# Kernel optimization log

Hardware: AMD Instinct MI355X
Metric: run time of the kernel (lower is better)

## Reference

```python
import jax, jax.numpy as jnp
import numpy as np

C, B, N, IN, OUT = 10, 128, 1152, 8, 16  # num_capsules, batch, num_route_nodes, in_ch, out_ch
NUM_ITERS = 3


def squash(t):
    # t: [..., OUT]
    sq_norm = jnp.sum(t * t, axis=-1, keepdims=True)
    scale = sq_norm / (1.0 + sq_norm)
    return scale * t / jnp.sqrt(sq_norm + 1e-8)


def setup_inputs() -> dict:
    key = jax.random.key(0)
    k1, k2 = jax.random.split(key)
    x = jax.random.normal(k1, (B, N, IN), dtype=jnp.float32)
    route_weights = jax.random.normal(k2, (C, N, IN, OUT), dtype=jnp.float32)
    return {"x": x, "route_weights": route_weights}


def reference(x, route_weights):
    # priors[c,b,n,o] = sum_i x[b,n,i] * W[c,n,i,o]
    priors = jnp.einsum('bni,cnio->cbno', x, route_weights)  # [C,B,N,OUT]
    # torch: logits = zeros_like(priors[:, :, :, 0]) -> [C,B,N,OUT] (dim 3 was the
    # singleton matmul row dim, so the OUT axis survives on the logits)
    logits = jnp.zeros_like(priors)
    outputs = None
    for _ in range(NUM_ITERS):
        attn = jax.nn.softmax(logits, axis=2)            # over route nodes N
        outputs = squash(jnp.sum(attn * priors, axis=2))  # [C,B,OUT]
        # (outputs * priors).sum(-1) broadcasts to [C,B,N,1] added to [C,B,N,OUT]
        logits = logits + jnp.sum(outputs[:, :, None, :] * priors, axis=-1, keepdims=True)
    return outputs  # [C,B,OUT] == outputs.squeeze() in torch (B>1, C>1)
```

## Files before the change

kernel.cpp:

```cpp
#include <hip/hip_runtime.h>
#include <hip/hip_bf16.h>


constexpr int C = 10, B = 128, N = 1152, IN = 8, OUT = 16;
constexpr int THREADS = 512;
constexpr int NW = THREADS / 64;
constexpr int G = 2;
constexpr int PASSES = N / (NW * 16);
constexpr int NBLK = C * (B / G);
constexpr int NXCD = 8;
constexpr int CHUNK = NBLK / NXCD;

__device__ __forceinline__ unsigned packbf(float a, float b) {
    __hip_bfloat162 h = __float22bfloat162_rn(float2{a, b});
    return *(unsigned*)&h;
}
__device__ __forceinline__ float bflo(unsigned u) { return __uint_as_float(u << 16); }
__device__ __forceinline__ float bfhi(unsigned u) { return __uint_as_float(u & 0xffff0000u); }

__global__ __launch_bounds__(THREADS)
void caps_route(const float* __restrict__ Xf, const float* __restrict__ Wf,
                float* __restrict__ Of) {
    __shared__ uint2 ldsP[G * PASSES * THREADS];
    __shared__ float lds_s[2][G][NW][OUT];
    __shared__ float lds_sum[2][G][NW];

    const int t = threadIdx.x;
    const int l = t & 63;
    const int wid = t >> 6;
    const int q = l & 3;
    const int rsub = l >> 2;

    const int bid = blockIdx.x;
    const int blk = (bid & (NXCD - 1)) * CHUNK + (bid >> 3);
    const int c = blk >> 6;
    const int b0 = (blk & 63) * G;

    #pragma unroll
    for (int p = 0; p < PASSES; ++p) {
        const int n = wid * (16 * PASSES) + p * 16 + rsub;
        const float4* wr = (const float4*)(Wf + (size_t)(c * N + n) * (IN * OUT));
        float4 wv[IN];
        #pragma unroll
        for (int i = 0; i < IN; ++i) wv[i] = wr[i * 4 + q];
        #pragma unroll
        for (int g = 0; g < G; ++g) {
            const float4* xr = (const float4*)(Xf + (size_t)((b0 + g) * N + n) * IN);
            const float4 xa = xr[0], xc = xr[1];
            const float xs[8] = { xa.x, xa.y, xa.z, xa.w, xc.x, xc.y, xc.z, xc.w };
            float a0 = 0.f, a1 = 0.f, a2 = 0.f, a3 = 0.f;
            #pragma unroll
            for (int i = 0; i < IN; ++i) {
                a0 = fmaf(xs[i], wv[i].x, a0);
                a1 = fmaf(xs[i], wv[i].y, a1);
                a2 = fmaf(xs[i], wv[i].z, a2);
                a3 = fmaf(xs[i], wv[i].w, a3);
            }
            ldsP[(g * PASSES + p) * THREADS + t] =
                uint2{packbf(a0, a1), packbf(a2, a3)};
        }
    }

    float oa[G][4];
    #pragma unroll
    for (int g = 0; g < G; ++g)
        #pragma unroll
        for (int k = 0; k < 4; ++k) oa[g][k] = 0.f;

    for (int it = 0; it < 3; ++it) {
        const int pb = it & 1;
        float s4[G][4];
        float ssum[G];
        if (it == 0) {
            #pragma unroll
            for (int g = 0; g < G; ++g) {
                ssum[g] = (float)PASSES;
                float a0 = 0.f, a1 = 0.f, a2 = 0.f, a3 = 0.f;
                #pragma unroll
                for (int p = 0; p < PASSES; ++p) {
                    const uint2 u = ldsP[(g * PASSES + p) * THREADS + t];
                    a0 += bflo(u.x); a1 += bfhi(u.x);
                    a2 += bflo(u.y); a3 += bfhi(u.y);
                }
                s4[g][0] = a0; s4[g][1] = a1; s4[g][2] = a2; s4[g][3] = a3;
            }
        } else {
            #pragma unroll
            for (int g = 0; g < G; ++g) {
                ssum[g] = 0.f;
                #pragma unroll
                for (int k = 0; k < 4; ++k) s4[g][k] = 0.f;
                #pragma unroll
                for (int p = 0; p < PASSES; ++p) {
                    const uint2 u = ldsP[(g * PASSES + p) * THREADS + t];
                    const float p0 = bflo(u.x), p1 = bfhi(u.x);
                    const float p2 = bflo(u.y), p3 = bfhi(u.y);
                    float d = oa[g][0] * p0;
                    d = fmaf(oa[g][1], p1, d);
                    d = fmaf(oa[g][2], p2, d);
                    d = fmaf(oa[g][3], p3, d);
                    d += __shfl_xor(d, 1, 64);
                    d += __shfl_xor(d, 2, 64);
                    const float e = __expf(d);
                    ssum[g] += e;
                    s4[g][0] = fmaf(e, p0, s4[g][0]);
                    s4[g][1] = fmaf(e, p1, s4[g][1]);
                    s4[g][2] = fmaf(e, p2, s4[g][2]);
                    s4[g][3] = fmaf(e, p3, s4[g][3]);
                }
            }
        }
        #pragma unroll
        for (int m = 4; m < 64; m <<= 1) {
            #pragma unroll
            for (int g = 0; g < G; ++g) {
                ssum[g] += __shfl_xor(ssum[g], m, 64);
                #pragma unroll
                for (int k = 0; k < 4; ++k) s4[g][k] += __shfl_xor(s4[g][k], m, 64);
            }
        }
        if (l < 4) {
            #pragma unroll
            for (int g = 0; g < G; ++g)
                #pragma unroll
                for (int k = 0; k < 4; ++k) lds_s[pb][g][wid][l * 4 + k] = s4[g][k];
        }
        if (l == 0) {
            #pragma unroll
            for (int g = 0; g < G; ++g) lds_sum[pb][g][wid] = ssum[g];
        }
        __syncthreads();

        float ov[G][4];
        #pragma unroll
        for (int g = 0; g < G; ++g) {
            float a0 = 0.f, a1 = 0.f, a2 = 0.f, a3 = 0.f, S = 0.f;
            #pragma unroll
            for (int w = 0; w < NW; ++w) {
                const float4 v = *(const float4*)&lds_s[pb][g][w][q * 4];
                a0 += v.x; a1 += v.y; a2 += v.z; a3 += v.w;
                S += lds_sum[pb][g][w];
            }
            const float inv = 1.f / S;
            const float s0 = a0 * inv, s1 = a1 * inv;
            const float s2 = a2 * inv, s3 = a3 * inv;
            float r = s0 * s0 + s1 * s1 + s2 * s2 + s3 * s3;
            r += __shfl_xor(r, 1, 64);
            r += __shfl_xor(r, 2, 64);
            const float sc = r / ((1.f + r) * sqrtf(r + 1e-8f));
            ov[g][0] = s0 * sc; ov[g][1] = s1 * sc;
            ov[g][2] = s2 * sc; ov[g][3] = s3 * sc;
        }
        if (it < 2) {
            #pragma unroll
            for (int g = 0; g < G; ++g)
                #pragma unroll
                for (int k = 0; k < 4; ++k) oa[g][k] += ov[g][k];
        } else if (t < 4) {
            #pragma unroll
            for (int g = 0; g < G; ++g)
                #pragma unroll
                for (int k = 0; k < 4; ++k)
                    Of[((size_t)c * B + b0 + g) * OUT + q * 4 + k] = ov[g][k];
        }
    }
}

extern "C" void kernel_launch(void* const* d_in, const int* in_sizes, int n_in,
                              void* d_out, int out_size, void* d_ws, size_t ws_size,
                              hipStream_t stream) {
    const float* X = (const float*)d_in[0];
    const float* W = (const float*)d_in[1];
    float* O = (float*)d_out;
    hipLaunchKernelGGL(caps_route, dim3(NBLK), dim3(THREADS), 0, stream, X, W, O);
}
```

Measured before the change: 94.95 us.

## Assign one batch element per block and fuse first-iteration sum into prior computation

Drops the two-batch-per-block grouping so each block handles one (capsule, batch) pair, doubling the grid and halving LDS per block. The first routing iteration's uniform sum is now accumulated in fp32 registers while priors are computed, so the LDS re-read pass is skipped. Launch bounds now request more resident blocks per CU. The trade-off is that each W row is loaded twice as often, once per batch element instead of once per pair.

After: 108.4 us. 1.14x slower.

```diff
diff --git a/kernel.cpp b/kernel.cpp
--- a/kernel.cpp
+++ b/kernel.cpp
@@ -5,9 +5,8 @@
 constexpr int C = 10, B = 128, N = 1152, IN = 8, OUT = 16;
 constexpr int THREADS = 512;
 constexpr int NW = THREADS / 64;
-constexpr int G = 2;
 constexpr int PASSES = N / (NW * 16);
-constexpr int NBLK = C * (B / G);
+constexpr int NBLK = C * B;
 constexpr int NXCD = 8;
 constexpr int CHUNK = NBLK / NXCD;
 
@@ -18,12 +17,12 @@
 __device__ __forceinline__ float bflo(unsigned u) { return __uint_as_float(u << 16); }
 __device__ __forceinline__ float bfhi(unsigned u) { return __uint_as_float(u & 0xffff0000u); }
 
-__global__ __launch_bounds__(THREADS)
+__global__ __launch_bounds__(THREADS, 8)
 void caps_route(const float* __restrict__ Xf, const float* __restrict__ Wf,
                 float* __restrict__ Of) {
-    __shared__ uint2 ldsP[G * PASSES * THREADS];
-    __shared__ float lds_s[2][G][NW][OUT];
-    __shared__ float lds_sum[2][G][NW];
+    __shared__ uint2 ldsP[PASSES * THREADS];
+    __shared__ float lds_s[2][NW][OUT];
+    __shared__ float lds_sum[2][NW];
 
     const int t = threadIdx.x;
     const int l = t & 63;
@@ -33,9 +32,10 @@
 
     const int bid = blockIdx.x;
     const int blk = (bid & (NXCD - 1)) * CHUNK + (bid >> 3);
-    const int c = blk >> 6;
-    const int b0 = (blk & 63) * G;
+    const int c = blk >> 7;
+    const int b = blk & 127;
 
+    float s40[4] = {0.f, 0.f, 0.f, 0.f};
     #pragma unroll
     for (int p = 0; p < PASSES; ++p) {
         const int n = wid * (16 * PASSES) + p * 16 + rsub;
@@ -43,125 +43,89 @@
         float4 wv[IN];
         #pragma unroll
         for (int i = 0; i < IN; ++i) wv[i] = wr[i * 4 + q];
+        const float4* xr = (const float4*)(Xf + (size_t)(b * N + n) * IN);
+        const float4 xa = xr[0], xc = xr[1];
+        const float xs[8] = { xa.x, xa.y, xa.z, xa.w, xc.x, xc.y, xc.z, xc.w };
+        float a0 = 0.f, a1 = 0.f, a2 = 0.f, a3 = 0.f;
         #pragma unroll
-        for (int g = 0; g < G; ++g) {
-            const float4* xr = (const float4*)(Xf + (size_t)((b0 + g) * N + n) * IN);
-            const float4 xa = xr[0], xc = xr[1];
-            const float xs[8] = { xa.x, xa.y, xa.z, xa.w, xc.x, xc.y, xc.z, xc.w };
-            float a0 = 0.f, a1 = 0.f, a2 = 0.f, a3 = 0.f;
-            #pragma unroll
-            for (int i = 0; i < IN; ++i) {
-                a0 = fmaf(xs[i], wv[i].x, a0);
-                a1 = fmaf(xs[i], wv[i].y, a1);
-                a2 = fmaf(xs[i], wv[i].z, a2);
-                a3 = fmaf(xs[i], wv[i].w, a3);
-            }
-            ldsP[(g * PASSES + p) * THREADS + t] =
-                uint2{packbf(a0, a1), packbf(a2, a3)};
+        for (int i = 0; i < IN; ++i) {
+            a0 = fmaf(xs[i], wv[i].x, a0);
+            a1 = fmaf(xs[i], wv[i].y, a1);
+            a2 = fmaf(xs[i], wv[i].z, a2);
+            a3 = fmaf(xs[i], wv[i].w, a3);
         }
+        s40[0] += a0; s40[1] += a1; s40[2] += a2; s40[3] += a3;
+        ldsP[p * THREADS + t] = uint2{packbf(a0, a1), packbf(a2, a3)};
     }
 
-    float oa[G][4];
-    #pragma unroll
-    for (int g = 0; g < G; ++g)
-        #pragma unroll
-        for (int k = 0; k < 4; ++k) oa[g][k] = 0.f;
+    float oa[4] = {0.f, 0.f, 0.f, 0.f};
 
     for (int it = 0; it < 3; ++it) {
         const int pb = it & 1;
-        float s4[G][4];
-        float ssum[G];
+        float s4[4];
+        float ssum;
         if (it == 0) {
+            ssum = (float)PASSES;
             #pragma unroll
-            for (int g = 0; g < G; ++g) {
-                ssum[g] = (float)PASSES;
-                float a0 = 0.f, a1 = 0.f, a2 = 0.f, a3 = 0.f;
-                #pragma unroll
-                for (int p = 0; p < PASSES; ++p) {
-                    const uint2 u = ldsP[(g * PASSES + p) * THREADS + t];
-                    a0 += bflo(u.x); a1 += bfhi(u.x);
-                    a2 += bflo(u.y); a3 += bfhi(u.y);
-                }
-                s4[g][0] = a0; s4[g][1] = a1; s4[g][2] = a2; s4[g][3] = a3;
-            }
+            for (int k = 0; k < 4; ++k) s4[k] = s40[k];
         } else {
+            ssum = 0.f;
             #pragma unroll
-            for (int g = 0; g < G; ++g) {
-                ssum[g] = 0.f;
-                #pragma unroll
-                for (int k = 0; k < 4; ++k) s4[g][k] = 0.f;
-                #pragma unroll
-                for (int p = 0; p < PASSES; ++p) {
-                    const uint2 u = ldsP[(g * PASSES + p) * THREADS + t];
-                    const float p0 = bflo(u.x), p1 = bfhi(u.x);
-                    const float p2 = bflo(u.y), p3 = bfhi(u.y);
-                    float d = oa[g][0] * p0;
-                    d = fmaf(oa[g][1], p1, d);
-                    d = fmaf(oa[g][2], p2, d);
-                    d = fmaf(oa[g][3], p3, d);
-                    d += __shfl_xor(d, 1, 64);
-                    d += __shfl_xor(d, 2, 64);
-                    const float e = __expf(d);
-                    ssum[g] += e;
-                    s4[g][0] = fmaf(e, p0, s4[g][0]);
-                    s4[g][1] = fmaf(e, p1, s4[g][1]);
-                    s4[g][2] = fmaf(e, p2, s4[g][2]);
-                    s4[g][3] = fmaf(e, p3, s4[g][3]);
-                }
+            for (int k = 0; k < 4; ++k) s4[k] = 0.f;
+            #pragma unroll
+            for (int p = 0; p < PASSES; ++p) {
+                const uint2 u = ldsP[p * THREADS + t];
+                const float p0 = bflo(u.x), p1 = bfhi(u.x);
+                const float p2 = bflo(u.y), p3 = bfhi(u.y);
+                float d = oa[0] * p0;
+                d = fmaf(oa[1], p1, d);
+                d = fmaf(oa[2], p2, d);
+                d = fmaf(oa[3], p3, d);
+                d += __shfl_xor(d, 1, 64);
+                d += __shfl_xor(d, 2, 64);
+                const float e = __expf(d);
+                ssum += e;
+                s4[0] = fmaf(e, p0, s4[0]);
+                s4[1] = fmaf(e, p1, s4[1]);
+                s4[2] = fmaf(e, p2, s4[2]);
+                s4[3] = fmaf(e, p3, s4[3]);
             }
         }
         #pragma unroll
         for (int m = 4; m < 64; m <<= 1) {
+            ssum += __shfl_xor(ssum, m, 64);
             #pragma unroll
-            for (int g = 0; g < G; ++g) {
-                ssum[g] += __shfl_xor(ssum[g], m, 64);
-                #pragma unroll
-                for (int k = 0; k < 4; ++k) s4[g][k] += __shfl_xor(s4[g][k], m, 64);
-            }
+            for (int k = 0; k < 4; ++k) s4[k] += __shfl_xor(s4[k], m, 64);
         }
         if (l < 4) {
             #pragma unroll
-            for (int g = 0; g < G; ++g)
-                #pragma unroll
-                for (int k = 0; k < 4; ++k) lds_s[pb][g][wid][l * 4 + k] = s4[g][k];
+            for (int k = 0; k < 4; ++k) lds_s[pb][wid][l * 4 + k] = s4[k];
         }
-        if (l == 0) {
-            #pragma unroll
-            for (int g = 0; g < G; ++g) lds_sum[pb][g][wid] = ssum[g];
-        }
+        if (l == 0) lds_sum[pb][wid] = ssum;
         __syncthreads();
 
-        float ov[G][4];
+        float a0 = 0.f, a1 = 0.f, a2 = 0.f, a3 = 0.f, S = 0.f;
         #pragma unroll
-        for (int g = 0; g < G; ++g) {
-            float a0 = 0.f, a1 = 0.f, a2 = 0.f, a3 = 0.f, S = 0.f;
-            #pragma unroll
-            for (int w = 0; w < NW; ++w) {
-                const float4 v = *(const float4*)&lds_s[pb][g][w][q * 4];
-                a0 += v.x; a1 += v.y; a2 += v.z; a3 += v.w;
-                S += lds_sum[pb][g][w];
-            }
-            const float inv = 1.f / S;
-            const float s0 = a0 * inv, s1 = a1 * inv;
-            const float s2 = a2 * inv, s3 = a3 * inv;
-            float r = s0 * s0 + s1 * s1 + s2 * s2 + s3 * s3;
-            r += __shfl_xor(r, 1, 64);
-            r += __shfl_xor(r, 2, 64);
-            const float sc = r / ((1.f + r) * sqrtf(r + 1e-8f));
-            ov[g][0] = s0 * sc; ov[g][1] = s1 * sc;
-            ov[g][2] = s2 * sc; ov[g][3] = s3 * sc;
+        for (int w = 0; w < NW; ++w) {
+            const float4 v = *(const float4*)&lds_s[pb][w][q * 4];
+            a0 += v.x; a1 += v.y; a2 += v.z; a3 += v.w;
+            S += lds_sum[pb][w];
         }
+        const float inv = 1.f / S;
+        const float s0 = a0 * inv, s1 = a1 * inv;
+        const float s2 = a2 * inv, s3 = a3 * inv;
+        float r = s0 * s0 + s1 * s1 + s2 * s2 + s3 * s3;
+        r += __shfl_xor(r, 1, 64);
+        r += __shfl_xor(r, 2, 64);
+        const float sc = r / ((1.f + r) * sqrtf(r + 1e-8f));
         if (it < 2) {
-            #pragma unroll
-            for (int g = 0; g < G; ++g)
-                #pragma unroll
-                for (int k = 0; k < 4; ++k) oa[g][k] += ov[g][k];
+            oa[0] += s0 * sc; oa[1] += s1 * sc;
+            oa[2] += s2 * sc; oa[3] += s3 * sc;
         } else if (t < 4) {
-            #pragma unroll
-            for (int g = 0; g < G; ++g)
-                #pragma unroll
-                for (int k = 0; k < 4; ++k)
-                    Of[((size_t)c * B + b0 + g) * OUT + q * 4 + k] = ov[g][k];
+            Of[((size_t)c * B + b) * OUT + q * 4 + 0] = s0 * sc;
+            Of[((size_t)c * B + b) * OUT + q * 4 + 1] = s1 * sc;
+            Of[((size_t)c * B + b) * OUT + q * 4 + 2] = s2 * sc;
+            Of[((size_t)c * B + b) * OUT + q * 4 + 3] = s3 * sc;
         }
     }
 }
```

## Use 1024-thread blocks with uneven row split and fused first-iteration sums

Applied to the files above, without the earlier changes.

Doubles the block size to 1024 threads (16 waves), so each wave now handles 72 route nodes in 4 or 5 row passes, with divergence on the last pass. The priors layout in LDS changes to node-major indexing. The first routing iteration's sums now come from fp32 accumulators during the priors computation, which skips one LDS re-read pass. The prior computation is also hand-interleaved for both batch rows and loads W in two halves to reduce register pressure. The risks are lower occupancy flexibility with 1024-thread blocks, divergence on the fifth pass, and a rolled loop.

After: 122.4 us. 1.29x slower.

```diff
diff --git a/kernel.cpp b/kernel.cpp
--- a/kernel.cpp
+++ b/kernel.cpp
@@ -3,10 +3,10 @@
 
 
 constexpr int C = 10, B = 128, N = 1152, IN = 8, OUT = 16;
-constexpr int THREADS = 512;
+constexpr int THREADS = 1024;
 constexpr int NW = THREADS / 64;
 constexpr int G = 2;
-constexpr int PASSES = N / (NW * 16);
+constexpr int ROWS_W = N / NW;
 constexpr int NBLK = C * (B / G);
 constexpr int NXCD = 8;
 constexpr int CHUNK = NBLK / NXCD;
@@ -21,7 +21,7 @@
 __global__ __launch_bounds__(THREADS)
 void caps_route(const float* __restrict__ Xf, const float* __restrict__ Wf,
                 float* __restrict__ Of) {
-    __shared__ uint2 ldsP[G * PASSES * THREADS];
+    __shared__ uint2 ldsP[G * N * 4];
     __shared__ float lds_s[2][G][NW][OUT];
     __shared__ float lds_sum[2][G][NW];
 
@@ -36,53 +36,70 @@
     const int c = blk >> 6;
     const int b0 = (blk & 63) * G;
 
-    #pragma unroll
-    for (int p = 0; p < PASSES; ++p) {
-        const int n = wid * (16 * PASSES) + p * 16 + rsub;
-        const float4* wr = (const float4*)(Wf + (size_t)(c * N + n) * (IN * OUT));
-        float4 wv[IN];
-        #pragma unroll
-        for (int i = 0; i < IN; ++i) wv[i] = wr[i * 4 + q];
-        #pragma unroll
-        for (int g = 0; g < G; ++g) {
-            const float4* xr = (const float4*)(Xf + (size_t)((b0 + g) * N + n) * IN);
-            const float4 xa = xr[0], xc = xr[1];
-            const float xs[8] = { xa.x, xa.y, xa.z, xa.w, xc.x, xc.y, xc.z, xc.w };
-            float a0 = 0.f, a1 = 0.f, a2 = 0.f, a3 = 0.f;
-            #pragma unroll
-            for (int i = 0; i < IN; ++i) {
-                a0 = fmaf(xs[i], wv[i].x, a0);
-                a1 = fmaf(xs[i], wv[i].y, a1);
-                a2 = fmaf(xs[i], wv[i].z, a2);
-                a3 = fmaf(xs[i], wv[i].w, a3);
-            }
-            ldsP[(g * PASSES + p) * THREADS + t] =
-                uint2{packbf(a0, a1), packbf(a2, a3)};
+    float s40[G][4] = {{0.f, 0.f, 0.f, 0.f}, {0.f, 0.f, 0.f, 0.f}};
+    const int nbase = wid * ROWS_W + rsub;
+    #pragma unroll 1
+    for (int p = 0; p < 5; ++p) {
+        if ((p < 4) | (rsub < 8)) {
+            const int n = nbase + p * 16;
+            const float4* wr = (const float4*)(Wf + (size_t)(c * N + n) * (IN * OUT)) + q;
+            const float4* x0 = (const float4*)(Xf + (size_t)((b0 + 0) * N + n) * IN);
+            const float4* x1 = (const float4*)(Xf + (size_t)((b0 + 1) * N + n) * IN);
+            const float4 xa0 = x0[0], xc0 = x0[1];
+            const float4 xa1 = x1[0], xc1 = x1[1];
+            float4 u0 = wr[0], u1 = wr[4], u2 = wr[8], u3 = wr[12];
+            float a0 = xa0.x * u0.x, a1 = xa0.x * u0.y, a2 = xa0.x * u0.z, a3 = xa0.x * u0.w;
+            float b0v = xa1.x * u0.x, b1v = xa1.x * u0.y, b2v = xa1.x * u0.z, b3v = xa1.x * u0.w;
+            a0 = fmaf(xa0.y, u1.x, a0); a1 = fmaf(xa0.y, u1.y, a1);
+            a2 = fmaf(xa0.y, u1.z, a2); a3 = fmaf(xa0.y, u1.w, a3);
+            b0v = fmaf(xa1.y, u1.x, b0v); b1v = fmaf(xa1.y, u1.y, b1v);
+            b2v = fmaf(xa1.y, u1.z, b2v); b3v = fmaf(xa1.y, u1.w, b3v);
+            a0 = fmaf(xa0.z, u2.x, a0); a1 = fmaf(xa0.z, u2.y, a1);
+            a2 = fmaf(xa0.z, u2.z, a2); a3 = fmaf(xa0.z, u2.w, a3);
+            b0v = fmaf(xa1.z, u2.x, b0v); b1v = fmaf(xa1.z, u2.y, b1v);
+            b2v = fmaf(xa1.z, u2.z, b2v); b3v = fmaf(xa1.z, u2.w, b3v);
+            a0 = fmaf(xa0.w, u3.x, a0); a1 = fmaf(xa0.w, u3.y, a1);
+            a2 = fmaf(xa0.w, u3.z, a2); a3 = fmaf(xa0.w, u3.w, a3);
+            b0v = fmaf(xa1.w, u3.x, b0v); b1v = fmaf(xa1.w, u3.y, b1v);
+            b2v = fmaf(xa1.w, u3.z, b2v); b3v = fmaf(xa1.w, u3.w, b3v);
+            u0 = wr[16]; u1 = wr[20]; u2 = wr[24]; u3 = wr[28];
+            a0 = fmaf(xc0.x, u0.x, a0); a1 = fmaf(xc0.x, u0.y, a1);
+            a2 = fmaf(xc0.x, u0.z, a2); a3 = fmaf(xc0.x, u0.w, a3);
+            b0v = fmaf(xc1.x, u0.x, b0v); b1v = fmaf(xc1.x, u0.y, b1v);
+            b2v = fmaf(xc1.x, u0.z, b2v); b3v = fmaf(xc1.x, u0.w, b3v);
+            a0 = fmaf(xc0.y, u1.x, a0); a1 = fmaf(xc0.y, u1.y, a1);
+            a2 = fmaf(xc0.y, u1.z, a2); a3 = fmaf(xc0.y, u1.w, a3);
+            b0v = fmaf(xc1.y, u1.x, b0v); b1v = fmaf(xc1.y, u1.y, b1v);
+            b2v = fmaf(xc1.y, u1.z, b2v); b3v = fmaf(xc1.y, u1.w, b3v);
+            a0 = fmaf(xc0.z, u2.x, a0); a1 = fmaf(xc0.z, u2.y, a1);
+            a2 = fmaf(xc0.z, u2.z, a2); a3 = fmaf(xc0.z, u2.w, a3);
+            b0v = fmaf(xc1.z, u2.x, b0v); b1v = fmaf(xc1.z, u2.y, b1v);
+            b2v = fmaf(xc1.z, u2.z, b2v); b3v = fmaf(xc1.z, u2.w, b3v);
+            a0 = fmaf(xc0.w, u3.x, a0); a1 = fmaf(xc0.w, u3.y, a1);
+            a2 = fmaf(xc0.w, u3.z, a2); a3 = fmaf(xc0.w, u3.w, a3);
+            b0v = fmaf(xc1.w, u3.x, b0v); b1v = fmaf(xc1.w, u3.y, b1v);
+            b2v = fmaf(xc1.w, u3.z, b2v); b3v = fmaf(xc1.w, u3.w, b3v);
+
+            s40[0][0] += a0;  s40[0][1] += a1;  s40[0][2] += a2;  s40[0][3] += a3;
+            s40[1][0] += b0v; s40[1][1] += b1v; s40[1][2] += b2v; s40[1][3] += b3v;
+            ldsP[(n << 2) | q]       = uint2{packbf(a0, a1), packbf(a2, a3)};
+            ldsP[((N + n) << 2) | q] = uint2{packbf(b0v, b1v), packbf(b2v, b3v)};
         }
     }
 
-    float oa[G][4];
-    #pragma unroll
-    for (int g = 0; g < G; ++g)
-        #pragma unroll
-        for (int k = 0; k < 4; ++k) oa[g][k] = 0.f;
+    float oa[G][4] = {{0.f, 0.f, 0.f, 0.f}, {0.f, 0.f, 0.f, 0.f}};
 
     for (int it = 0; it < 3; ++it) {
         const int pb = it & 1;
         float s4[G][4];
         float ssum[G];
         if (it == 0) {
+            const float rows = (rsub < 8) ? 5.f : 4.f;
             #pragma unroll
             for (int g = 0; g < G; ++g) {
-                ssum[g] = (float)PASSES;
-                float a0 = 0.f, a1 = 0.f, a2 = 0.f, a3 = 0.f;
+                ssum[g] = rows;
                 #pragma unroll
-                for (int p = 0; p < PASSES; ++p) {
-                    const uint2 u = ldsP[(g * PASSES + p) * THREADS + t];
-                    a0 += bflo(u.x); a1 += bfhi(u.x);
-                    a2 += bflo(u.y); a3 += bfhi(u.y);
-                }
-                s4[g][0] = a0; s4[g][1] = a1; s4[g][2] = a2; s4[g][3] = a3;
+                for (int k = 0; k < 4; ++k) s4[g][k] = s40[g][k];
             }
         } else {
             #pragma unroll
@@ -90,23 +107,29 @@
                 ssum[g] = 0.f;
                 #pragma unroll
                 for (int k = 0; k < 4; ++k) s4[g][k] = 0.f;
-                #pragma unroll
-                for (int p = 0; p < PASSES; ++p) {
-                    const uint2 u = ldsP[(g * PASSES + p) * THREADS + t];
-                    const float p0 = bflo(u.x), p1 = bfhi(u.x);
-                    const float p2 = bflo(u.y), p3 = bfhi(u.y);
-                    float d = oa[g][0] * p0;
-                    d = fmaf(oa[g][1], p1, d);
-                    d = fmaf(oa[g][2], p2, d);
-                    d = fmaf(oa[g][3], p3, d);
-                    d += __shfl_xor(d, 1, 64);
-                    d += __shfl_xor(d, 2, 64);
-                    const float e = __expf(d);
-                    ssum[g] += e;
-                    s4[g][0] = fmaf(e, p0, s4[g][0]);
-                    s4[g][1] = fmaf(e, p1, s4[g][1]);
-                    s4[g][2] = fmaf(e, p2, s4[g][2]);
-                    s4[g][3] = fmaf(e, p3, s4[g][3]);
+            }
+            #pragma unroll
+            for (int p = 0; p < 5; ++p) {
+                if ((p < 4) | (rsub < 8)) {
+                    const int n = nbase + p * 16;
+                    #pragma unroll
+                    for (int g = 0; g < G; ++g) {
+                        const uint2 u = ldsP[((g * N + n) << 2) | q];
+                        const float p0 = bflo(u.x), p1 = bfhi(u.x);
+                        const float p2 = bflo(u.y), p3 = bfhi(u.y);
+                        float d = oa[g][0] * p0;
+                        d = fmaf(oa[g][1], p1, d);
+                        d = fmaf(oa[g][2], p2, d);
+                        d = fmaf(oa[g][3], p3, d);
+                        d += __shfl_xor(d, 1, 64);
+                        d += __shfl_xor(d, 2, 64);
+                        const float e = __expf(d);
+                        ssum[g] += e;
+                        s4[g][0] = fmaf(e, p0, s4[g][0]);
+                        s4[g][1] = fmaf(e, p1, s4[g][1]);
+                        s4[g][2] = fmaf(e, p2, s4[g][2]);
+                        s4[g][3] = fmaf(e, p3, s4[g][3]);
+                    }
                 }
             }
         }
```
